# Kernel optimization log

Measured on AMD Instinct MI355X. Metric: run time of the kernel, lower is better.

## Reference

```python
import jax, jax.numpy as jnp
import numpy as np

IN_FEATURES = 256
OUT_FEATURES = 256
GRID_SIZE = 5
SPLINE_ORDER = 3
GRID_RANGE = (-1.0, 1.0)
LN_EPS = 1e-5


def _make_grid():
    h = (GRID_RANGE[1] - GRID_RANGE[0]) / GRID_SIZE
    n_knots = GRID_SIZE + 2 * SPLINE_ORDER + 1  # 12
    return jnp.linspace(GRID_RANGE[0] - h * SPLINE_ORDER,
                        GRID_RANGE[1] + h * SPLINE_ORDER,
                        n_knots, dtype=jnp.float32)


def setup_inputs() -> dict:
    key = jax.random.key(0)
    k1, k2, k3 = jax.random.split(key, 3)
    N = 65536
    # kaiming_uniform_(nonlinearity='linear'): bound = sqrt(3/fan_in)
    b1 = np.sqrt(3.0 / IN_FEATURES)
    fan_sp = IN_FEATURES * (GRID_SIZE + SPLINE_ORDER)
    b2 = np.sqrt(3.0 / fan_sp)
    return {
        "x": jax.random.normal(k1, (N, IN_FEATURES), dtype=jnp.float32),
        "grid": _make_grid(),
        "base_weight": jax.random.uniform(k2, (OUT_FEATURES, IN_FEATURES), jnp.float32, -b1, b1),
        "spline_weight": jax.random.uniform(k3, (OUT_FEATURES, IN_FEATURES, GRID_SIZE + SPLINE_ORDER), jnp.float32, -b2, b2),
        "ln_gamma": jnp.ones((OUT_FEATURES,), jnp.float32),
        "ln_beta": jnp.zeros((OUT_FEATURES,), jnp.float32),
        "prelu_a": jnp.full((1,), 0.25, jnp.float32),
    }


def reference(x, grid, base_weight, spline_weight, ln_gamma, ln_beta, prelu_a):
    # base branch: exact GELU then linear (matches nn.GELU() + F.linear)
    base_out = jnp.einsum('ni,oi->no', jax.nn.gelu(x, approximate=False), base_weight)

    # Cox-de Boor B-spline basis recursion. grid is identical per feature in
    # the original ([in, 12] expand of a 1D linspace) so we broadcast the 1D grid.
    xu = x[:, :, None]                                   # [N, in, 1]
    bases = ((xu >= grid[:-1]) & (xu < grid[1:])).astype(x.dtype)  # [N, in, 11]
    for k in range(1, SPLINE_ORDER + 1):
        left = grid[:-(k + 1)]
        right = grid[k:-1]
        delta = jnp.where(right == left, jnp.ones_like(right), right - left)
        bases = ((xu - left) / delta * bases[:, :, :-1]
                 + (grid[k + 1:] - xu) / (grid[k + 1:] - grid[1:-k]) * bases[:, :, 1:])
    # bases: [N, in, grid_size + spline_order]

    spline_out = jnp.einsum('nig,oig->no', bases, spline_weight)

    y = base_out + spline_out
    mu = jnp.mean(y, axis=-1, keepdims=True)
    var = jnp.mean(jnp.square(y - mu), axis=-1, keepdims=True)
    y = (y - mu) * jax.lax.rsqrt(var + LN_EPS) * ln_gamma + ln_beta
    # PReLU with a single shared slope (nn.PReLU default)
    return jnp.where(y >= 0, y, prelu_a[0] * y)
```

## Files before the change

kernel.cpp:

```cpp
#include <hip/hip_runtime.h>
#include <hip/hip_bf16.h>
#include <math.h>
#include <stdint.h>

typedef __attribute__((ext_vector_type(8))) short short8;
typedef __attribute__((ext_vector_type(4))) float f32x4;

#define BM 256
#define NKT 36
#define A_BYTES (BM * 128)
#define LDS_TOTAL (4 * A_BYTES)

__device__ __forceinline__ unsigned short f2bf(float f) {
    __bf16 h = (__bf16)f;
    return __builtin_bit_cast(unsigned short, h);
}

__device__ __forceinline__ float gelu_exact(float x) {
    return 0.5f * x * (1.0f + erff(x * 0.7071067811865475f));
}

__device__ __forceinline__ int swz(int row, int u) {
    return row * 128 + ((u ^ (row & 7)) << 4);
}

__global__ void kan_prep_w(const float* __restrict__ bw, const float* __restrict__ sw,
                           unsigned short* __restrict__ Wf) {
    int U = blockIdx.x * 256 + threadIdx.x;
    if (U >= NKT * 2048) return;
    int kt = U >> 11, rem = U & 2047;
    int wcq = rem >> 9, rem2 = rem & 511;
    int i = rem2 >> 6;
    int lane = rem2 & 63;
    int o = wcq * 64 + (i & 3) * 16 + (lane & 15);
    int k0 = kt * 64 + ((i >> 2) * 4 + (lane >> 4)) * 8;
    unsigned short pk[8];
#pragma unroll
    for (int e = 0; e < 8; ++e) {
        int kk = k0 + e;
        float v = (kk < 256) ? bw[o * 256 + kk] : sw[o * 2048 + (kk - 256)];
        pk[e] = f2bf(v);
    }
    *(short8*)(Wf + (size_t)U * 8) = *(short8*)pk;
}

__device__ __forceinline__ short8 spline_row(float xv) {
    float xi = (xv + 2.2f) * 2.5f;
    float fi = floorf(xi);
    float tt = xi - fi;
    float s1 = 1.0f - tt;
    float t2 = tt * tt, t3 = t2 * tt;
    float w0 = s1 * s1 * s1 * (1.0f / 6.0f);
    float w1 = 0.5f * t3 - t2 + (2.0f / 3.0f);
    float w2 = -0.5f * t3 + 0.5f * t2 + 0.5f * tt + (1.0f / 6.0f);
    float w3 = t3 * (1.0f / 6.0f);
    uint64_t Wp = (uint64_t)f2bf(w0) | ((uint64_t)f2bf(w1) << 16)
                | ((uint64_t)f2bf(w2) << 32) | ((uint64_t)f2bf(w3) << 48);
    int b = 16 * ((int)fi - 3);
    uint64_t L = (b >= 0 && b < 64) ? (Wp << b)
               : ((b < 0 && b > -64) ? (Wp >> (-b)) : 0ull);
    uint64_t H = (b >= 64 && b < 128) ? (Wp << (b - 64))
               : ((b > 0 && b < 64) ? (Wp >> (64 - b)) : 0ull);
    union { uint64_t q[2]; short8 v; } rr;
    rr.q[0] = L; rr.q[1] = H;
    return rr.v;
}

__global__ __launch_bounds__(512)
void kan_fused(
    const float* __restrict__ X, const unsigned short* __restrict__ Wf,
    const float* __restrict__ gamma, const float* __restrict__ beta,
    const float* __restrict__ prelu_a, float* __restrict__ OUT)
{
    extern __shared__ __align__(16) unsigned char lds[];

    const int t = threadIdx.x;
    const int row0 = blockIdx.x * BM;
    const int wid = t >> 6, lane = t & 63;
    const int wr = wid >> 2, wc = wid & 3;
    const int lcol = lane & 15, q = lane >> 4;
    const int srow = t >> 3, scol = t & 7;

    f32x4 acc[8][4];
#pragma unroll
    for (int m = 0; m < 8; ++m)
#pragma unroll
        for (int n = 0; n < 4; ++n) acc[m][n] = (f32x4){0.f, 0.f, 0.f, 0.f};

    const unsigned short* wlane = Wf + ((size_t)wc * 512 + lane) * 8;
    short8 wv[8];

    auto w_load = [&](int kt) {
        const unsigned short* wsrc = wlane + (size_t)kt * 2048 * 8;
#pragma unroll
        for (int i = 0; i < 8; ++i)
            wv[i] = *(const short8*)(wsrc + i * 512);
    };
    auto gelu_stage = [&](int kt, unsigned char* D) {
#pragma unroll
        for (int rep = 0; rep < 4; ++rep) {
            const float* xp = X + (size_t)(row0 + srow + rep * 64) * 256 + kt * 64 + scol * 8;
            float4 v0 = *(const float4*)xp;
            float4 v1 = *(const float4*)(xp + 4);
            float vv[8] = {v0.x, v0.y, v0.z, v0.w, v1.x, v1.y, v1.z, v1.w};
            unsigned short pk[8];
#pragma unroll
            for (int jj = 0; jj < 8; ++jj) pk[jj] = f2bf(gelu_exact(vv[jj]));
            *(short8*)(D + swz(srow + rep * 64, scol)) = *(short8*)pk;
        }
    };
    auto spline_stage = [&](float (&xs)[4], unsigned char* D) {
#pragma unroll
        for (int rep = 0; rep < 4; ++rep)
            *(short8*)(D + swz(srow + rep * 64, scol)) = spline_row(xs[rep]);
    };
    auto mfma_tile = [&](unsigned char* B) {
#pragma unroll
        for (int kh = 0; kh < 2; ++kh) {
            short8 af[8];
#pragma unroll
            for (int m = 0; m < 8; ++m)
                af[m] = *(const short8*)(B + swz(wr * 128 + m * 16 + lcol, kh * 4 + q));
#pragma unroll
            for (int m = 0; m < 8; ++m)
#pragma unroll
                for (int n = 0; n < 4; ++n)
                    acc[m][n] = __builtin_amdgcn_mfma_f32_16x16x32_bf16(
                        af[m], wv[kh * 4 + n], acc[m][n], 0, 0, 0);
        }
    };

    w_load(0);
    gelu_stage(0, lds);
    gelu_stage(1, lds + A_BYTES);
    asm volatile("s_waitcnt lgkmcnt(0)\n\ts_barrier" ::: "memory");

    for (int j = 0; j < NKT / 2; ++j) {
        const int ka = 2 * j, kb = ka + 1;
        unsigned char* Ba = lds + (ka & 3) * A_BYTES;
        unsigned char* Bb = lds + (kb & 3) * A_BYTES;
        unsigned char* Sa = lds + ((ka + 2) & 3) * A_BYTES;
        unsigned char* Sb = lds + ((ka + 3) & 3) * A_BYTES;
        const bool stg = (ka + 2 < NKT);
        const bool gA = (ka + 2 < 4), gB = (ka + 3 < 4);

        float xsA[4], xsB[4];
        if (stg && !gA) {
            const int ibA = (ka + 2 - 4) * 8;
#pragma unroll
            for (int rep = 0; rep < 4; ++rep)
                xsA[rep] = X[(size_t)(row0 + srow + rep * 64) * 256 + ibA + scol];
        }
        if (stg && !gB) {
            const int ibB = (ka + 3 - 4) * 8;
#pragma unroll
            for (int rep = 0; rep < 4; ++rep)
                xsB[rep] = X[(size_t)(row0 + srow + rep * 64) * 256 + ibB + scol];
        }

        mfma_tile(Ba);
        w_load(kb);
        if (stg) { if (gA) gelu_stage(ka + 2, Sa); else spline_stage(xsA, Sa); }
        mfma_tile(Bb);
        if (ka + 2 < NKT) w_load(ka + 2);
        if (stg) { if (gB) gelu_stage(ka + 3, Sb); else spline_stage(xsB, Sb); }

        asm volatile("s_waitcnt lgkmcnt(0)\n\ts_barrier" ::: "memory");
    }

    float* stats = (float*)lds;
#pragma unroll
    for (int m = 0; m < 8; ++m) {
#pragma unroll
        for (int r = 0; r < 4; ++r) {
            float s = 0.f, s2 = 0.f;
#pragma unroll
            for (int n = 0; n < 4; ++n) { float v = acc[m][n][r]; s += v; s2 += v * v; }
#pragma unroll
            for (int msk = 1; msk < 16; msk <<= 1) {
                s  += __shfl_xor(s,  msk, 64);
                s2 += __shfl_xor(s2, msk, 64);
            }
            if ((lane & 15) == ((m * 4 + r) & 15)) {
                int row = wr * 128 + m * 16 + q * 4 + r;
                stats[row * 8 + wc]     = s;
                stats[row * 8 + 4 + wc] = s2;
            }
        }
    }
    __syncthreads();

    const float apr = prelu_a[0];
    float gv[4], bv[4];
#pragma unroll
    for (int n = 0; n < 4; ++n) {
        int col = wc * 64 + n * 16 + lcol;
        gv[n] = gamma[col]; bv[n] = beta[col];
    }
#pragma unroll
    for (int m = 0; m < 8; ++m) {
#pragma unroll
        for (int r = 0; r < 4; ++r) {
            int row = wr * 128 + m * 16 + q * 4 + r;
            f32x4 sv = *(const f32x4*)(stats + row * 8);
            f32x4 qv = *(const f32x4*)(stats + row * 8 + 4);
            float mu  = (sv[0] + sv[1] + sv[2] + sv[3]) * (1.0f / 256.0f);
            float ex2 = (qv[0] + qv[1] + qv[2] + qv[3]) * (1.0f / 256.0f);
            float rs = rsqrtf(ex2 - mu * mu + 1e-5f);
            float* op = OUT + (size_t)(row0 + row) * 256;
#pragma unroll
            for (int n = 0; n < 4; ++n) {
                int col = wc * 64 + n * 16 + lcol;
                float y = (acc[m][n][r] - mu) * rs * gv[n] + bv[n];
                op[col] = (y >= 0.f) ? y : apr * y;
            }
        }
    }
}

extern "C" void kernel_launch(void* const* d_in, const int* in_sizes, int n_in,
                              void* d_out, int out_size, void* d_ws, size_t ws_size,
                              hipStream_t stream) {
    const float* x  = (const float*)d_in[0];
    const float* bw = (const float*)d_in[2];
    const float* sw = (const float*)d_in[3];
    const float* g  = (const float*)d_in[4];
    const float* be = (const float*)d_in[5];
    const float* pa = (const float*)d_in[6];
    float* out = (float*)d_out;
    unsigned short* Wf = (unsigned short*)d_ws;

    hipFuncSetAttribute((const void*)kan_fused,
                        hipFuncAttributeMaxDynamicSharedMemorySize, LDS_TOTAL);

    const int Nrows = in_sizes[0] / 256;
    kan_prep_w<<<(NKT * 2048 + 255) / 256, 256, 0, stream>>>(bw, sw, Wf);
    kan_fused<<<Nrows / BM, 512, LDS_TOTAL, stream>>>(x, Wf, g, be, pa, out);
}
```

Baseline: 126.5 us.

## Double block to 1024 threads with smaller per-wave tiles and inline weight loads

Raises the fused kernel to 16 waves per 256-row block, so each wave accumulates a 64x64 tile instead of 128x64, which halves the accumulator registers per wave. Weight fragments are now fetched inside the MFMA tile from a re-laid-out packed buffer (8 contiguous short8 per lane) instead of being software-prefetched one tile ahead. The staging work per thread is halved to match. More waves give more latency hiding, but weights are reloaded by twice as many waves and the removed prefetch may expose global-load latency before each MFMA.

```diff
diff --git a/kernel.cpp b/kernel.cpp
--- a/kernel.cpp
+++ b/kernel.cpp
@@ -30,10 +30,10 @@
     if (U >= NKT * 2048) return;
     int kt = U >> 11, rem = U & 2047;
     int wcq = rem >> 9, rem2 = rem & 511;
-    int i = rem2 >> 6;
-    int lane = rem2 & 63;
-    int o = wcq * 64 + (i & 3) * 16 + (lane & 15);
-    int k0 = kt * 64 + ((i >> 2) * 4 + (lane >> 4)) * 8;
+    int lane = rem2 >> 3, i = rem2 & 7;
+    int n = i & 3, kh = i >> 2;
+    int o = wcq * 64 + n * 16 + (lane & 15);
+    int k0 = kt * 64 + (kh * 4 + (lane >> 4)) * 8;
     unsigned short pk[8];
 #pragma unroll
     for (int e = 0; e < 8; ++e) {
@@ -66,7 +66,7 @@
     return rr.v;
 }
 
-__global__ __launch_bounds__(512)
+__global__ __launch_bounds__(1024)
 void kan_fused(
     const float* __restrict__ X, const unsigned short* __restrict__ Wf,
     const float* __restrict__ gamma, const float* __restrict__ beta,
@@ -79,90 +79,84 @@
     const int wid = t >> 6, lane = t & 63;
     const int wr = wid >> 2, wc = wid & 3;
     const int lcol = lane & 15, q = lane >> 4;
-    const int srow = t >> 3, scol = t & 7;
-
-    f32x4 acc[8][4];
-#pragma unroll
-    for (int m = 0; m < 8; ++m)
+    const int srow = t >> 2, sil = (t & 3) << 1;
+
+    f32x4 acc[4][4];
+#pragma unroll
+    for (int m = 0; m < 4; ++m)
 #pragma unroll
         for (int n = 0; n < 4; ++n) acc[m][n] = (f32x4){0.f, 0.f, 0.f, 0.f};
 
-    const unsigned short* wlane = Wf + ((size_t)wc * 512 + lane) * 8;
-    short8 wv[8];
-
-    auto w_load = [&](int kt) {
-        const unsigned short* wsrc = wlane + (size_t)kt * 2048 * 8;
-#pragma unroll
-        for (int i = 0; i < 8; ++i)
-            wv[i] = *(const short8*)(wsrc + i * 512);
+    const short8* wp = (const short8*)(Wf + ((size_t)wc * 512 + lane * 8) * 8);
+
+    auto mfma_tile = [&](unsigned char* B) {
+#pragma unroll
+        for (int kh = 0; kh < 2; ++kh) {
+            short8 wv4[4];
+#pragma unroll
+            for (int n = 0; n < 4; ++n) wv4[n] = wp[kh * 4 + n];
+            short8 af[4];
+#pragma unroll
+            for (int m = 0; m < 4; ++m)
+                af[m] = *(const short8*)(B + swz(wr * 64 + m * 16 + lcol, kh * 4 + q));
+#pragma unroll
+            for (int m = 0; m < 4; ++m)
+#pragma unroll
+                for (int n = 0; n < 4; ++n)
+                    acc[m][n] = __builtin_amdgcn_mfma_f32_16x16x32_bf16(
+                        af[m], wv4[n], acc[m][n], 0, 0, 0);
+        }
+        wp += 2048;
+    };
+    auto spline_stage = [&](float (&xs)[2], unsigned char* D) {
+#pragma unroll
+        for (int rep = 0; rep < 2; ++rep)
+            *(short8*)(D + swz(srow, sil + rep)) = spline_row(xs[rep]);
     };
     auto gelu_stage = [&](int kt, unsigned char* D) {
 #pragma unroll
-        for (int rep = 0; rep < 4; ++rep) {
-            const float* xp = X + (size_t)(row0 + srow + rep * 64) * 256 + kt * 64 + scol * 8;
+        for (int rep = 0; rep < 2; ++rep) {
+            const float* xp = X + (size_t)(row0 + srow) * 256 + kt * 64 + (sil + rep) * 8;
             float4 v0 = *(const float4*)xp;
             float4 v1 = *(const float4*)(xp + 4);
             float vv[8] = {v0.x, v0.y, v0.z, v0.w, v1.x, v1.y, v1.z, v1.w};
             unsigned short pk[8];
 #pragma unroll
             for (int jj = 0; jj < 8; ++jj) pk[jj] = f2bf(gelu_exact(vv[jj]));
-            *(short8*)(D + swz(srow + rep * 64, scol)) = *(short8*)pk;
+            *(short8*)(D + swz(srow, sil + rep)) = *(short8*)pk;
         }
     };
-    auto spline_stage = [&](float (&xs)[4], unsigned char* D) {
-#pragma unroll
-        for (int rep = 0; rep < 4; ++rep)
-            *(short8*)(D + swz(srow + rep * 64, scol)) = spline_row(xs[rep]);
-    };
-    auto mfma_tile = [&](unsigned char* B) {
-#pragma unroll
-        for (int kh = 0; kh < 2; ++kh) {
-            short8 af[8];
-#pragma unroll
-            for (int m = 0; m < 8; ++m)
-                af[m] = *(const short8*)(B + swz(wr * 128 + m * 16 + lcol, kh * 4 + q));
-#pragma unroll
-            for (int m = 0; m < 8; ++m)
-#pragma unroll
-                for (int n = 0; n < 4; ++n)
-                    acc[m][n] = __builtin_amdgcn_mfma_f32_16x16x32_bf16(
-                        af[m], wv[kh * 4 + n], acc[m][n], 0, 0, 0);
-        }
-    };
-
-    w_load(0);
+
     gelu_stage(0, lds);
     gelu_stage(1, lds + A_BYTES);
     asm volatile("s_waitcnt lgkmcnt(0)\n\ts_barrier" ::: "memory");
 
     for (int j = 0; j < NKT / 2; ++j) {
-        const int ka = 2 * j, kb = ka + 1;
+        const int ka = 2 * j;
         unsigned char* Ba = lds + (ka & 3) * A_BYTES;
-        unsigned char* Bb = lds + (kb & 3) * A_BYTES;
+        unsigned char* Bb = lds + ((ka + 1) & 3) * A_BYTES;
         unsigned char* Sa = lds + ((ka + 2) & 3) * A_BYTES;
         unsigned char* Sb = lds + ((ka + 3) & 3) * A_BYTES;
         const bool stg = (ka + 2 < NKT);
         const bool gA = (ka + 2 < 4), gB = (ka + 3 < 4);
 
-        float xsA[4], xsB[4];
+        float xsA[2], xsB[2];
         if (stg && !gA) {
             const int ibA = (ka + 2 - 4) * 8;
 #pragma unroll
-            for (int rep = 0; rep < 4; ++rep)
-                xsA[rep] = X[(size_t)(row0 + srow + rep * 64) * 256 + ibA + scol];
+            for (int rep = 0; rep < 2; ++rep)
+                xsA[rep] = X[(size_t)(row0 + srow) * 256 + ibA + sil + rep];
         }
         if (stg && !gB) {
             const int ibB = (ka + 3 - 4) * 8;
 #pragma unroll
-            for (int rep = 0; rep < 4; ++rep)
-                xsB[rep] = X[(size_t)(row0 + srow + rep * 64) * 256 + ibB + scol];
+            for (int rep = 0; rep < 2; ++rep)
+                xsB[rep] = X[(size_t)(row0 + srow) * 256 + ibB + sil + rep];
         }
 
         mfma_tile(Ba);
-        w_load(kb);
         if (stg) { if (gA) gelu_stage(ka + 2, Sa); else spline_stage(xsA, Sa); }
         mfma_tile(Bb);
-        if (ka + 2 < NKT) w_load(ka + 2);
         if (stg) { if (gB) gelu_stage(ka + 3, Sb); else spline_stage(xsB, Sb); }
 
         asm volatile("s_waitcnt lgkmcnt(0)\n\ts_barrier" ::: "memory");
@@ -170,7 +164,7 @@
 
     float* stats = (float*)lds;
 #pragma unroll
-    for (int m = 0; m < 8; ++m) {
+    for (int m = 0; m < 4; ++m) {
 #pragma unroll
         for (int r = 0; r < 4; ++r) {
             float s = 0.f, s2 = 0.f;
@@ -181,8 +175,8 @@
                 s  += __shfl_xor(s,  msk, 64);
                 s2 += __shfl_xor(s2, msk, 64);
             }
-            if ((lane & 15) == ((m * 4 + r) & 15)) {
-                int row = wr * 128 + m * 16 + q * 4 + r;
+            if ((lane & 15) == (m * 4 + r)) {
+                int row = wr * 64 + m * 16 + q * 4 + r;
                 stats[row * 8 + wc]     = s;
                 stats[row * 8 + 4 + wc] = s2;
             }
@@ -198,10 +192,10 @@
         gv[n] = gamma[col]; bv[n] = beta[col];
     }
 #pragma unroll
-    for (int m = 0; m < 8; ++m) {
+    for (int m = 0; m < 4; ++m) {
 #pragma unroll
         for (int r = 0; r < 4; ++r) {
-            int row = wr * 128 + m * 16 + q * 4 + r;
+            int row = wr * 64 + m * 16 + q * 4 + r;
             f32x4 sv = *(const f32x4*)(stats + row * 8);
             f32x4 qv = *(const f32x4*)(stats + row * 8 + 4);
             float mu  = (sv[0] + sv[1] + sv[2] + sv[3]) * (1.0f / 256.0f);
@@ -235,5 +229,5 @@
 
     const int Nrows = in_sizes[0] / 256;
     kan_prep_w<<<(NKT * 2048 + 255) / 256, 256, 0, stream>>>(bw, sw, Wf);
-    kan_fused<<<Nrows / BM, 512, LDS_TOTAL, stream>>>(x, Wf, g, be, pa, out);
-}
+    kan_fused<<<Nrows / BM, 1024, LDS_TOTAL, stream>>>(x, Wf, g, be, pa, out);
+}
```

Measured after the change: 218.2 us. +72.5%, slower.
